# Kernel optimization log

Hardware: AMD Instinct MI355X
Metric: run time of the kernel (lower is better)

Reference implementation:

```python
import jax, jax.numpy as jnp
import numpy as np

B, T, N, K, IB, O = 128, 16, 65536, 8, 256, 10

def setup_inputs() -> dict:
    key = jax.random.key(0)
    ks = jax.random.split(key, 8)
    x = jax.random.randint(ks[0], (B, T, IB), 0, 2, dtype=jnp.int32)          # boolean input bits per timestep
    adj_list = jax.random.randint(ks[1], (N, K), 0, N, dtype=jnp.int32)       # incoming neighbors, homogenized
    adj_mask = jnp.ones((N, K), dtype=jnp.int32)                               # validity mask (all valid here)
    lut = jax.random.randint(ks[2], (N, 2 ** K), 0, 2, dtype=jnp.int32)        # boolean lookup table per node
    init_state = jax.random.randint(ks[3], (N,), 0, 2, dtype=jnp.int32)        # 'random' init strategy
    w_in = jnp.arange(IB, dtype=jnp.int32)                                     # input-bit -> node index map
    w_readout = jax.random.normal(ks[4], (O, N), dtype=jnp.float32) * 0.01
    b_readout = jax.random.normal(ks[5], (O,), dtype=jnp.float32)
    return dict(x=x, adj_list=adj_list, adj_mask=adj_mask, lut=lut,
                init_state=init_state, w_in=w_in,
                w_readout=w_readout, b_readout=b_readout)

def _run_reservoir(x, adj_list, adj_mask, lut, init_state, w_in):
    # x: [B,T,IB] bits; returns final boolean state [B,N] (int32)
    powers = (2 ** jnp.arange(K, dtype=jnp.int32))[::-1]   # matches powers_of_2 flip
    node_idx = jnp.arange(N, dtype=jnp.int32)
    state0 = jnp.broadcast_to(init_state[None, :], (B, N)).astype(jnp.int32)

    def step(state, xt):
        # perturb input nodes with this timestep's bits (xor perturbation)
        state = state.at[:, w_in].set(jnp.bitwise_xor(state[:, w_in], xt))
        # gather incoming-neighbor states, mask padded slots: [B,N,K]
        neigh = jnp.take(state, adj_list, axis=1) * adj_mask
        # pack K bits into LUT index, MSB-first: [B,N]
        idx = jnp.sum(neigh * powers, axis=-1)
        # per-node boolean update via LUT gather
        new_state = lut[node_idx[None, :], idx]
        return new_state, None

    xT = jnp.swapaxes(x, 0, 1)  # [T,B,IB]
    final, _ = jax.lax.scan(step, state0, xT)
    return final

def reference(x, adj_list, adj_mask, lut, init_state, w_in, w_readout, b_readout):
    final = _run_reservoir(x, adj_list, adj_mask, lut, init_state, w_in)
    logits = final.astype(jnp.float32) @ w_readout.T + b_readout  # [B,O]
    return jax.nn.sigmoid(logits)
```

## Files before the change

### kernel.cpp

```cpp
#include <hip/hip_runtime.h>
#include <stdint.h>

#define NN     65536
#define KK     8
#define BB     128
#define TT     16
#define IBITS  256
#define OO     10

#define ZIDX         (NN + IBITS)
#define SBUF_ENTRIES (NN + IBITS + 1)
#define RCHUNKS 512
#define RNODES  128

__device__ __forceinline__ uint32_t bmask(uint32_t w, int off) {
  return (uint32_t)__builtin_amdgcn_sbfe((int)w, off, 1);
}
__device__ __forceinline__ uint32_t mux(uint32_t s, uint32_t hi, uint32_t lo) {
  return ((hi ^ lo) & s) ^ lo;
}

template<int D, int BASE> struct Sh1 {
  static __device__ __forceinline__ uint32_t eval(const uint32_t (&L)[8],
                                                  const uint32_t (&xv)[8]) {
    uint32_t lo = Sh1<D - 1, BASE>::eval(L, xv);
    uint32_t hi = Sh1<D - 1, BASE + (1 << (D - 1))>::eval(L, xv);
    return mux(xv[D - 1], hi, lo);
  }
};
template<int BASE> struct Sh1<2, BASE> {
  static __device__ __forceinline__ uint32_t eval(const uint32_t (&L)[8],
                                                  const uint32_t (&xv)[8]) {
    const uint32_t lw = L[BASE >> 5];
    const uint32_t c0 = bmask(lw, (BASE & 31) + 0);
    const uint32_t c1 = bmask(lw, (BASE & 31) + 1);
    const uint32_t c2 = bmask(lw, (BASE & 31) + 2);
    const uint32_t c3 = bmask(lw, (BASE & 31) + 3);
    const uint32_t t0 = mux(xv[0], c1, c0);
    const uint32_t t1 = mux(xv[0], c3, c2);
    return mux(xv[1], t1, t0);
  }
};

#define PB_LUT   2048
#define PB_MADJ  2048
#define PB_X     64
#define PB_STATE 256
#define PREP_BLOCKS (PB_LUT + PB_MADJ + PB_X + PB_STATE)

__global__ __launch_bounds__(256) void prep_kernel(
    const int* __restrict__ lut, const int* __restrict__ adj,
    const int* __restrict__ adjm, const int* __restrict__ x,
    const int* __restrict__ init,
    uint32_t* __restrict__ luttt, int* __restrict__ madj,
    uint32_t* __restrict__ xvecw, uint4* __restrict__ sA, uint4* __restrict__ sB) {
  const int b = blockIdx.x, t = threadIdx.x;
  if (b < PB_LUT) {
    const int g = b * 256 + t;
    const int n = g >> 3, w = g & 7;
    const int4* lut4 = (const int4*)lut;
    uint32_t val = 0;
#pragma unroll
    for (int q = 0; q < 8; ++q) {
      int4 v = lut4[n * 64 + w * 8 + q];
      val |= (uint32_t)(v.x & 1) << (4 * q + 0);
      val |= (uint32_t)(v.y & 1) << (4 * q + 1);
      val |= (uint32_t)(v.z & 1) << (4 * q + 2);
      val |= (uint32_t)(v.w & 1) << (4 * q + 3);
    }
    luttt[g] = val;
  } else if (b < PB_LUT + PB_MADJ) {
    const int g = (b - PB_LUT) * 256 + t;
    int a = adj[g];
    int m = adjm[g] & 1;
    madj[g] = m ? ((a < IBITS) ? a + NN : a) : ZIDX;
  } else if (b < PB_LUT + PB_MADJ + PB_X) {
    const int g = (b - PB_LUT - PB_MADJ) * 256 + t;
    const int tt = g >> 10, rest = g & 1023, i = rest >> 2, bq = rest & 3;
    uint32_t wv = 0;
#pragma unroll
    for (int bl = 0; bl < 32; ++bl) {
      int bb = bq * 32 + bl;
      wv |= (uint32_t)(x[(bb * TT + tt) * IBITS + i] & 1) << bl;
    }
    xvecw[(tt * IBITS + i) * 4 + bq] = wv;
  } else {
    const int n = (b - PB_LUT - PB_MADJ - PB_X) * 256 + t;
    uint32_t m = 0u - (uint32_t)(init[n] & 1);
    uint4 s = make_uint4(m, m, m, m);
    sA[n] = s;
    if (n < IBITS) {
      uint32_t wv[4] = {0, 0, 0, 0};
#pragma unroll
      for (int bb = 0; bb < BB; ++bb) {
        uint32_t bit = (uint32_t)(x[(bb * TT + 0) * IBITS + n] & 1);
        wv[bb >> 5] |= bit << (bb & 31);
      }
      sA[NN + n] = make_uint4(s.x ^ wv[0], s.y ^ wv[1], s.z ^ wv[2], s.w ^ wv[3]);
    }
    if (n == 0) {
      uint4 z = make_uint4(0, 0, 0, 0);
      sA[ZIDX] = z;
      sB[ZIDX] = z;
    }
  }
}

__global__ __launch_bounds__(256) void step_kernel(const uint32_t* __restrict__ sinw,
                                                   uint32_t* __restrict__ soutw,
                                                   const uint4* __restrict__ luttt,
                                                   const int* __restrict__ madj,
                                                   const uint32_t* __restrict__ xnextw) {
  const int g = blockIdx.x * 256 + threadIdx.x;
  const int n = g >> 2, w = g & 3;
  const int4* madj4 = (const int4*)madj;
  int4 a0 = madj4[n * 2 + 0], a1 = madj4[n * 2 + 1];
  uint4 l0 = luttt[n * 2 + 0], l1 = luttt[n * 2 + 1];
  const int ia[8] = {a0.x, a0.y, a0.z, a0.w, a1.x, a1.y, a1.z, a1.w};
  uint32_t xv[8];
#pragma unroll
  for (int k = 7; k >= 0; --k) {
    xv[7 - k] = sinw[(ia[k] << 2) + w];
  }
  const uint32_t L[8] = {l0.x, l0.y, l0.z, l0.w, l1.x, l1.y, l1.z, l1.w};
  uint32_t r = Sh1<8, 0>::eval(L, xv);
  soutw[(n << 2) + w] = r;
  if (xnextw != nullptr && n < IBITS) {
    soutw[((NN + n) << 2) + w] = r ^ xnextw[(n << 2) + w];
  }
}

__global__ __launch_bounds__(256) void readout_kernel(const uint32_t* __restrict__ statew,
                                                      const float* __restrict__ w,
                                                      float* __restrict__ part) {
  __shared__ uint32_t sw[64 * 4];
  __shared__ float wsm[OO * 64];
  const int c = blockIdx.x;
  const int t = threadIdx.x;
  const int b = t & 127, oh = t >> 7;
  const int word = b >> 5, sh = b & 31;
  float acc[5] = {0.f, 0.f, 0.f, 0.f, 0.f};
  for (int s = 0; s < 2; ++s) {
    const int base = c * RNODES + s * 64;
    __syncthreads();
    sw[t] = statew[base * 4 + t];
#pragma unroll
    for (int r = 0; r < 3; ++r) {
      int idx = r * 256 + t;
      if (idx < OO * 64) wsm[idx] = w[(idx >> 6) * NN + base + (idx & 63)];
    }
    __syncthreads();
#pragma unroll 8
    for (int j = 0; j < 64; ++j) {
      uint32_t m = 0u - ((sw[j * 4 + word] >> sh) & 1u);
#pragma unroll
      for (int q = 0; q < 5; ++q) {
        uint32_t wv = __float_as_uint(wsm[(oh * 5 + q) * 64 + j]) & m;
        acc[q] += __uint_as_float(wv);
      }
    }
  }
#pragma unroll
  for (int q = 0; q < 5; ++q)
    part[(c * BB + b) * OO + oh * 5 + q] = acc[q];
}

__global__ __launch_bounds__(256) void finalize_kernel(const float* __restrict__ part,
                                                       const float* __restrict__ bias,
                                                       float* __restrict__ out) {
  __shared__ float red[256];
  const int i = blockIdx.x;
  const int b = i / OO, o = i % OO;
  const int t = threadIdx.x;
  float s = part[(t * BB + b) * OO + o] + part[((t + 256) * BB + b) * OO + o];
  red[t] = s;
  __syncthreads();
  for (int h = 128; h > 0; h >>= 1) {
    if (t < h) red[t] += red[t + h];
    __syncthreads();
  }
  if (t == 0) out[b * OO + o] = 1.f / (1.f + __expf(-(red[0] + bias[o])));
}

extern "C" void kernel_launch(void* const* d_in, const int* in_sizes, int n_in,
                              void* d_out, int out_size, void* d_ws, size_t ws_size,
                              hipStream_t stream) {
  const int* x    = (const int*)d_in[0];
  const int* adj  = (const int*)d_in[1];
  const int* adjm = (const int*)d_in[2];
  const int* lut  = (const int*)d_in[3];
  const int* init = (const int*)d_in[4];
  const float* wro = (const float*)d_in[6];
  const float* bro = (const float*)d_in[7];
  float* out = (float*)d_out;

  char* ws = (char*)d_ws;
  const size_t SBUF = (size_t)SBUF_ENTRIES * 16;
  uint4* sA        = (uint4*)(ws);
  uint4* sB        = (uint4*)(ws + SBUF);
  uint32_t* xvecw  = (uint32_t*)(ws + 2 * SBUF);
  uint32_t* luttt  = (uint32_t*)(ws + 2 * SBUF + (size_t)TT * IBITS * 16);
  int* madj        = (int*)(ws + 2 * SBUF + (size_t)TT * IBITS * 16 + (size_t)NN * 32);
  float* part      = (float*)(ws + 2 * SBUF + (size_t)TT * IBITS * 16 + (size_t)NN * 64);

  hipLaunchKernelGGL(prep_kernel, dim3(PREP_BLOCKS), dim3(256), 0, stream,
                     lut, adj, adjm, x, init, luttt, madj, xvecw, sA, sB);

  for (int t = 0; t < TT; ++t) {
    const uint32_t* sin = (const uint32_t*)((t & 1) ? sB : sA);
    uint32_t* sout      = (uint32_t*)((t & 1) ? sA : sB);
    const uint32_t* xn  = (t + 1 < TT) ? (xvecw + (size_t)(t + 1) * IBITS * 4) : nullptr;
    hipLaunchKernelGGL(step_kernel, dim3((NN * 4) / 256), dim3(256), 0, stream,
                       sin, sout, (const uint4*)luttt, madj, xn);
  }
  hipLaunchKernelGGL(readout_kernel, dim3(RCHUNKS), dim3(256), 0, stream,
                     (const uint32_t*)sA, wro, part);
  hipLaunchKernelGGL(finalize_kernel, dim3(BB * OO), dim3(256), 0, stream, part, bro, out);
}
```

Baseline: 287.9 us.

## Split each node's LUT mux tree across two lanes with shuffle combine

Each node-word is now handled by two threads: each evaluates a 7-input mux tree over half of the 256-entry LUT, and the two halves are combined through a lane shuffle and a final mux on the MSB input. This doubles thread count, halves per-thread LUT loads and ALU depth, and sets launch bounds for higher occupancy. In exchange, every neighbor-state gather is done twice, once per lane of the pair, which adds memory traffic and launch work.

```diff
diff --git a/kernel.cpp b/kernel.cpp
--- a/kernel.cpp
+++ b/kernel.cpp
@@ -20,17 +20,17 @@
   return ((hi ^ lo) & s) ^ lo;
 }
 
-template<int D, int BASE> struct Sh1 {
-  static __device__ __forceinline__ uint32_t eval(const uint32_t (&L)[8],
-                                                  const uint32_t (&xv)[8]) {
-    uint32_t lo = Sh1<D - 1, BASE>::eval(L, xv);
-    uint32_t hi = Sh1<D - 1, BASE + (1 << (D - 1))>::eval(L, xv);
+template<int D, int BASE> struct Sh7 {
+  static __device__ __forceinline__ uint32_t eval(const uint32_t (&L)[4],
+                                                  const uint32_t (&xv)[7]) {
+    uint32_t lo = Sh7<D - 1, BASE>::eval(L, xv);
+    uint32_t hi = Sh7<D - 1, BASE + (1 << (D - 1))>::eval(L, xv);
     return mux(xv[D - 1], hi, lo);
   }
 };
-template<int BASE> struct Sh1<2, BASE> {
-  static __device__ __forceinline__ uint32_t eval(const uint32_t (&L)[8],
-                                                  const uint32_t (&xv)[8]) {
+template<int BASE> struct Sh7<2, BASE> {
+  static __device__ __forceinline__ uint32_t eval(const uint32_t (&L)[4],
+                                                  const uint32_t (&xv)[7]) {
     const uint32_t lw = L[BASE >> 5];
     const uint32_t c0 = bmask(lw, (BASE & 31) + 0);
     const uint32_t c1 = bmask(lw, (BASE & 31) + 1);
@@ -106,26 +106,33 @@
   }
 }
 
-__global__ __launch_bounds__(256) void step_kernel(const uint32_t* __restrict__ sinw,
-                                                   uint32_t* __restrict__ soutw,
-                                                   const uint4* __restrict__ luttt,
-                                                   const int* __restrict__ madj,
-                                                   const uint32_t* __restrict__ xnextw) {
+__global__ __launch_bounds__(256, 8) void step_kernel(const uint32_t* __restrict__ sinw,
+                                                      uint32_t* __restrict__ soutw,
+                                                      const uint4* __restrict__ luttt,
+                                                      const int* __restrict__ madj,
+                                                      const uint32_t* __restrict__ xnextw) {
   const int g = blockIdx.x * 256 + threadIdx.x;
-  const int n = g >> 2, w = g & 3;
+  const int n = g >> 3;
+  const int w = (g >> 1) & 3;
+  const int h = g & 1;
   const int4* madj4 = (const int4*)madj;
   int4 a0 = madj4[n * 2 + 0], a1 = madj4[n * 2 + 1];
-  uint4 l0 = luttt[n * 2 + 0], l1 = luttt[n * 2 + 1];
+  uint4 lh = luttt[n * 2 + h];
+  const uint32_t L[4] = {lh.x, lh.y, lh.z, lh.w};
   const int ia[8] = {a0.x, a0.y, a0.z, a0.w, a1.x, a1.y, a1.z, a1.w};
-  uint32_t xv[8];
-#pragma unroll
-  for (int k = 7; k >= 0; --k) {
-    xv[7 - k] = sinw[(ia[k] << 2) + w];
-  }
-  const uint32_t L[8] = {l0.x, l0.y, l0.z, l0.w, l1.x, l1.y, l1.z, l1.w};
-  uint32_t r = Sh1<8, 0>::eval(L, xv);
-  soutw[(n << 2) + w] = r;
-  if (xnextw != nullptr && n < IBITS) {
+  uint32_t xv[7];
+#pragma unroll
+  for (int j = 0; j < 7; ++j)
+    xv[j] = sinw[(ia[7 - j] << 2) + w];
+  const uint32_t x7 = sinw[(ia[0] << 2) + w];
+  const uint32_t rsub = Sh7<7, 0>::eval(L, xv);
+  const uint32_t rpart = __shfl_xor(rsub, 1, 64);
+  const uint32_t lo = h ? rpart : rsub;
+  const uint32_t hi = h ? rsub : rpart;
+  const uint32_t r = mux(x7, hi, lo);
+  if (h == 0) {
+    soutw[(n << 2) + w] = r;
+  } else if (xnextw != nullptr && n < IBITS) {
     soutw[((NN + n) << 2) + w] = r ^ xnextw[(n << 2) + w];
   }
 }
@@ -210,7 +217,7 @@
     const uint32_t* sin = (const uint32_t*)((t & 1) ? sB : sA);
     uint32_t* sout      = (uint32_t*)((t & 1) ? sA : sB);
     const uint32_t* xn  = (t + 1 < TT) ? (xvecw + (size_t)(t + 1) * IBITS * 4) : nullptr;
-    hipLaunchKernelGGL(step_kernel, dim3((NN * 4) / 256), dim3(256), 0, stream,
+    hipLaunchKernelGGL(step_kernel, dim3((NN * 8) / 256), dim3(256), 0, stream,
                        sin, sout, (const uint4*)luttt, madj, xn);
   }
   hipLaunchKernelGGL(readout_kernel, dim3(RCHUNKS), dim3(256), 0, stream,
```

Result: no change. 288.4 us (+0.2%).
